# Kernel tuning notes

Measured on AMD Instinct MI355X. Metric: run time of the kernel, lower is better.

Reference implementation:

```python
import jax, jax.numpy as jnp
import numpy as np


def setup_inputs() -> dict:
    key = jax.random.key(0)
    k1, k2 = jax.random.split(key)
    N, I, J, K = 256, 32, 32, 256
    x = jax.random.normal(k1, (N, I, K), dtype=jnp.float32)
    z = jax.random.normal(k2, (N, J, K), dtype=jnp.float32)
    return {"x": x, "z": z}


def reference(x, z):
    # Original torch code loops over batch rolls; rolling only permutes the set
    # over which log_softmax (a permutation-invariant logsumexp) is taken, and
    # index 0 of the roll stack is always the diagonal pair (x[n], z[n]).
    # So it is exactly a symmetric InfoNCE over the full pairwise score matrix.
    J = z.shape[1]
    # Full pairwise token-level similarity: [N_x, N_z, I, J]
    sim = jnp.einsum('aik,bjk->abij', x, z)
    # score(x_a, z_b) = sum_{i,j} softmax_i(sim)*sim / J
    w = jax.nn.softmax(sim, axis=2) * sim
    S = w.sum(axis=(2, 3)) / J  # [N_x, N_z]
    diag = jnp.diagonal(S)
    # loss_x[n] = -log_softmax over x-candidates (axis 0) at the diagonal
    loss_x = jax.nn.logsumexp(S, axis=0) - diag
    # loss_z[n] = -log_softmax over z-candidates (axis 1) at the diagonal
    loss_z = jax.nn.logsumexp(S, axis=1) - diag
    loss = loss_x + loss_z
    return loss.mean()  # reduction='mean'
```

## Files before the change

kernel.cpp:

```cpp
#include <hip/hip_runtime.h>
#include <hip/hip_bf16.h>
#include <stdint.h>


typedef __attribute__((ext_vector_type(8))) short short8;
typedef __attribute__((ext_vector_type(16))) float float16;

#define NTOK 256
#define KDIM 256

__device__ __forceinline__ unsigned short f2bf(float f) {
    unsigned int u = __float_as_uint(f);
    unsigned int r = (u + 0x7fffu + ((u >> 16) & 1u)) >> 16;
    return (unsigned short)r;
}

__device__ __forceinline__ short8 cvt8(const float* p) {
    float4 f0 = ((const float4*)p)[0];
    float4 f1 = ((const float4*)p)[1];
    short8 v;
    v[0] = (short)f2bf(f0.x); v[1] = (short)f2bf(f0.y);
    v[2] = (short)f2bf(f0.z); v[3] = (short)f2bf(f0.w);
    v[4] = (short)f2bf(f1.x); v[5] = (short)f2bf(f1.y);
    v[6] = (short)f2bf(f1.z); v[7] = (short)f2bf(f1.w);
    return v;
}

__global__ void conv_kernel(const float* __restrict__ x,
                            const float* __restrict__ z,
                            short8* __restrict__ outbf,
                            float* __restrict__ out0) {
    const int uid = blockIdx.x * 256 + threadIdx.x;
    if (uid == 0) out0[0] = 0.0f;
    const int u = uid & 262143;
    const float* src = (uid < 262144) ? x : z;
    const int g  = u >> 10;
    const int r  = u & 1023;
    const int ks = r >> 6;
    const int h  = (r >> 5) & 1;
    const int l  = r & 31;
    outbf[uid] = cvt8(src + ((g * 32 + l) * KDIM + ks * 16 + h * 8));
}

template <bool F32SRC>
__global__ __launch_bounds__(256, 4)
void sim_kernel(const short8* __restrict__ xbf, const short8* __restrict__ zbf,
                const float* __restrict__ xf, const float* __restrict__ zf,
                float* __restrict__ S) {
    const int tid  = threadIdx.x;
    const int lane = tid & 63;
    const int wid  = tid >> 6;
    const int aw   = wid >> 1;
    const int bw   = wid & 1;
    const int l31  = lane & 31;
    const int half = lane >> 5;
    const int bid  = blockIdx.x;
    const int a0   = (bid >> 6) * 4;
    const int b0   = (bid & 63) * 4;

    const int ag = a0 + 2 * aw;
    const int bg = b0 + 2 * bw;

    const short8* pa = xbf + ag * 1024 + lane;
    const short8* pb = zbf + bg * 1024 + lane;

    const float* fa = xf + ((ag * 32 + l31) * KDIM + half * 8);
    const float* fb = zf + ((bg * 32 + l31) * KDIM + half * 8);

    float16 acc[2][2];
#pragma unroll
    for (int ai = 0; ai < 2; ai++)
#pragma unroll
        for (int bi = 0; bi < 2; bi++)
#pragma unroll
            for (int r = 0; r < 16; r++) acc[ai][bi][r] = 0.0f;

#pragma unroll 4
    for (int ks = 0; ks < 16; ks++) {
        short8 a0f, a1f, b0f, b1f;
        if (F32SRC) {
            a0f = cvt8(fa + ks * 16);
            a1f = cvt8(fa + 32 * KDIM + ks * 16);
            b0f = cvt8(fb + ks * 16);
            b1f = cvt8(fb + 32 * KDIM + ks * 16);
        } else {
            const int off = ks * 64;
            a0f = pa[off];
            a1f = pa[off + 1024];
            b0f = pb[off];
            b1f = pb[off + 1024];
        }
        acc[0][0] = __builtin_amdgcn_mfma_f32_32x32x16_bf16(a0f, b0f, acc[0][0], 0, 0, 0);
        acc[0][1] = __builtin_amdgcn_mfma_f32_32x32x16_bf16(a0f, b1f, acc[0][1], 0, 0, 0);
        acc[1][0] = __builtin_amdgcn_mfma_f32_32x32x16_bf16(a1f, b0f, acc[1][0], 0, 0, 0);
        acc[1][1] = __builtin_amdgcn_mfma_f32_32x32x16_bf16(a1f, b1f, acc[1][1], 0, 0, 0);
    }

#pragma unroll
    for (int ai = 0; ai < 2; ai++) {
#pragma unroll
        for (int bi = 0; bi < 2; bi++) {
            float16 c = acc[ai][bi];
            float m = c[0];
#pragma unroll
            for (int r = 1; r < 16; r++) m = fmaxf(m, c[r]);
            m = fmaxf(m, __shfl_xor(m, 32, 64));
            float se = 0.0f, swe = 0.0f;
#pragma unroll
            for (int r = 0; r < 16; r++) {
                float e = __expf(c[r] - m);
                se += e;
                swe = fmaf(e, c[r], swe);
            }
            se  += __shfl_xor(se, 32, 64);
            swe += __shfl_xor(swe, 32, 64);
            float cv = swe / se;
#pragma unroll
            for (int off = 1; off < 32; off <<= 1) cv += __shfl_xor(cv, off, 64);
            if (lane == 0)
                S[(ag + ai) * NTOK + (bg + bi)] = cv * (1.0f / 32.0f);
        }
    }
}

__global__ void loss_part(const float* __restrict__ S, float* __restrict__ out) {
    const int lane = threadIdx.x & 63;
    const int wid  = threadIdx.x >> 6;
    const int n    = blockIdx.x * 4 + wid;

    float cv[4], rv[4];
#pragma unroll
    for (int k = 0; k < 4; k++) {
        const int t = lane + 64 * k;
        cv[k] = S[t * NTOK + n];
        rv[k] = S[n * NTOK + t];
    }
    float m = fmaxf(fmaxf(cv[0], cv[1]), fmaxf(cv[2], cv[3]));
#pragma unroll
    for (int off = 1; off < 64; off <<= 1) m = fmaxf(m, __shfl_xor(m, off, 64));
    float s = 0.0f;
#pragma unroll
    for (int k = 0; k < 4; k++) s += __expf(cv[k] - m);
#pragma unroll
    for (int off = 1; off < 64; off <<= 1) s += __shfl_xor(s, off, 64);
    float lse_col = m + __logf(s);

    float m2 = fmaxf(fmaxf(rv[0], rv[1]), fmaxf(rv[2], rv[3]));
#pragma unroll
    for (int off = 1; off < 64; off <<= 1) m2 = fmaxf(m2, __shfl_xor(m2, off, 64));
    float s2 = 0.0f;
#pragma unroll
    for (int k = 0; k < 4; k++) s2 += __expf(rv[k] - m2);
#pragma unroll
    for (int off = 1; off < 64; off <<= 1) s2 += __shfl_xor(s2, off, 64);
    float lse_row = m2 + __logf(s2);

    __shared__ float red[4];
    if (lane == 0) {
        float diag = S[n * NTOK + n];
        red[wid] = (lse_col - diag) + (lse_row - diag);
    }
    __syncthreads();
    if (threadIdx.x == 0)
        atomicAdd(out, (red[0] + red[1] + red[2] + red[3]) * (1.0f / 256.0f));
}

__global__ void zero_kernel(float* __restrict__ out) {
    out[0] = 0.0f;
}

extern "C" void kernel_launch(void* const* d_in, const int* in_sizes, int n_in,
                              void* d_out, int out_size, void* d_ws, size_t ws_size,
                              hipStream_t stream) {
    const float* x = (const float*)d_in[0];
    const float* z = (const float*)d_in[1];
    float* out = (float*)d_out;

    const size_t bf_bytes = 524288ull * 16ull;
    const size_t s_bytes  = 256ull * 256ull * 4ull;

    if (ws_size >= bf_bytes + s_bytes) {
        short8* xbf = (short8*)d_ws;
        short8* zbf = xbf + 262144;
        float*  S   = (float*)((char*)d_ws + bf_bytes);
        conv_kernel<<<2048, 256, 0, stream>>>(x, z, (short8*)d_ws, out);
        sim_kernel<false><<<4096, 256, 0, stream>>>(xbf, zbf, nullptr, nullptr, S);
        loss_part<<<64, 256, 0, stream>>>(S, out);
    } else {
        float* S = (float*)d_ws;
        zero_kernel<<<1, 1, 0, stream>>>(out);
        sim_kernel<true><<<4096, 256, 0, stream>>>(nullptr, nullptr, x, z, S);
        loss_part<<<64, 256, 0, stream>>>(S, out);
    }
}
```

Before: 117.9 us.

## Defer cross-lane score reduction to a separate fp16 partial-sum kernel

Result: no change. 120.0 us (+1.8%).

```diff
diff --git a/kernel.cpp b/kernel.cpp
--- a/kernel.cpp
+++ b/kernel.cpp
@@ -1,5 +1,6 @@
 #include <hip/hip_runtime.h>
 #include <hip/hip_bf16.h>
+#include <hip/hip_fp16.h>
 #include <stdint.h>
 
 
@@ -42,11 +43,77 @@
     outbf[uid] = cvt8(src + ((g * 32 + l) * KDIM + ks * 16 + h * 8));
 }
 
-template <bool F32SRC>
+__device__ __forceinline__ void tile_epilogue_sp(const float16& c, __half* __restrict__ Sp,
+                                                 int a, int b, int lane) {
+    float m8[8], m4[4];
+#pragma unroll
+    for (int r = 0; r < 8; r++) m8[r] = fmaxf(c[2 * r], c[2 * r + 1]);
+#pragma unroll
+    for (int r = 0; r < 4; r++) m4[r] = fmaxf(m8[2 * r], m8[2 * r + 1]);
+    float m = fmaxf(fmaxf(m4[0], m4[1]), fmaxf(m4[2], m4[3]));
+    m = fmaxf(m, __shfl_xor(m, 32, 64));
+
+    float s0 = 0.f, s1 = 0.f, s2 = 0.f, s3 = 0.f;
+    float w0 = 0.f, w1 = 0.f, w2 = 0.f, w3 = 0.f;
+#pragma unroll
+    for (int r = 0; r < 16; r += 4) {
+        float e0 = __expf(c[r + 0] - m);
+        float e1 = __expf(c[r + 1] - m);
+        float e2 = __expf(c[r + 2] - m);
+        float e3 = __expf(c[r + 3] - m);
+        s0 += e0; s1 += e1; s2 += e2; s3 += e3;
+        w0 = fmaf(e0, c[r + 0], w0);
+        w1 = fmaf(e1, c[r + 1], w1);
+        w2 = fmaf(e2, c[r + 2], w2);
+        w3 = fmaf(e3, c[r + 3], w3);
+    }
+    float se  = (s0 + s1) + (s2 + s3);
+    float swe = (w0 + w1) + (w2 + w3);
+    se  += __shfl_xor(se, 32, 64);
+    swe += __shfl_xor(swe, 32, 64);
+    float cv = swe * __builtin_amdgcn_rcpf(se);
+    Sp[(((a << 8) + b) << 6) + lane] = __float2half_rn(cv);
+}
+
+__device__ __forceinline__ void tile_epilogue_bf(const float16& c, float* __restrict__ S,
+                                                 int a, int b, int lane) {
+    float m8[8], m4[4];
+#pragma unroll
+    for (int r = 0; r < 8; r++) m8[r] = fmaxf(c[2 * r], c[2 * r + 1]);
+#pragma unroll
+    for (int r = 0; r < 4; r++) m4[r] = fmaxf(m8[2 * r], m8[2 * r + 1]);
+    float m = fmaxf(fmaxf(m4[0], m4[1]), fmaxf(m4[2], m4[3]));
+    m = fmaxf(m, __shfl_xor(m, 32, 64));
+
+    float s0 = 0.f, s1 = 0.f, s2 = 0.f, s3 = 0.f;
+    float w0 = 0.f, w1 = 0.f, w2 = 0.f, w3 = 0.f;
+#pragma unroll
+    for (int r = 0; r < 16; r += 4) {
+        float e0 = __expf(c[r + 0] - m);
+        float e1 = __expf(c[r + 1] - m);
+        float e2 = __expf(c[r + 2] - m);
+        float e3 = __expf(c[r + 3] - m);
+        s0 += e0; s1 += e1; s2 += e2; s3 += e3;
+        w0 = fmaf(e0, c[r + 0], w0);
+        w1 = fmaf(e1, c[r + 1], w1);
+        w2 = fmaf(e2, c[r + 2], w2);
+        w3 = fmaf(e3, c[r + 3], w3);
+    }
+    float se  = (s0 + s1) + (s2 + s3);
+    float swe = (w0 + w1) + (w2 + w3);
+    se  += __shfl_xor(se, 32, 64);
+    swe += __shfl_xor(swe, 32, 64);
+    float cv = swe * __builtin_amdgcn_rcpf(se);
+#pragma unroll
+    for (int off = 1; off < 32; off <<= 1) cv += __shfl_xor(cv, off, 64);
+    if (lane == 0) S[a * NTOK + b] = cv * (1.0f / 32.0f);
+}
+
+template <bool F32SRC, bool SPSTORE>
 __global__ __launch_bounds__(256, 4)
 void sim_kernel(const short8* __restrict__ xbf, const short8* __restrict__ zbf,
                 const float* __restrict__ xf, const float* __restrict__ zf,
-                float* __restrict__ S) {
+                __half* __restrict__ Sp, float* __restrict__ S) {
     const int tid  = threadIdx.x;
     const int lane = tid & 63;
     const int wid  = tid >> 6;
@@ -97,30 +164,24 @@
     }
 
 #pragma unroll
-    for (int ai = 0; ai < 2; ai++) {
+    for (int ai = 0; ai < 2; ai++)
 #pragma unroll
         for (int bi = 0; bi < 2; bi++) {
-            float16 c = acc[ai][bi];
-            float m = c[0];
-#pragma unroll
-            for (int r = 1; r < 16; r++) m = fmaxf(m, c[r]);
-            m = fmaxf(m, __shfl_xor(m, 32, 64));
-            float se = 0.0f, swe = 0.0f;
-#pragma unroll
-            for (int r = 0; r < 16; r++) {
-                float e = __expf(c[r] - m);
-                se += e;
-                swe = fmaf(e, c[r], swe);
-            }
-            se  += __shfl_xor(se, 32, 64);
-            swe += __shfl_xor(swe, 32, 64);
-            float cv = swe / se;
-#pragma unroll
-            for (int off = 1; off < 32; off <<= 1) cv += __shfl_xor(cv, off, 64);
-            if (lane == 0)
-                S[(ag + ai) * NTOK + (bg + bi)] = cv * (1.0f / 32.0f);
+            if (SPSTORE) tile_epilogue_sp(acc[ai][bi], Sp, ag + ai, bg + bi, lane);
+            else         tile_epilogue_bf(acc[ai][bi], S,  ag + ai, bg + bi, lane);
         }
-    }
+}
+
+__global__ void red_kernel(const __half* __restrict__ Sp, float* __restrict__ S) {
+    const int t = blockIdx.x * 256 + threadIdx.x;
+    const __half2* h2 = (const __half2*)(Sp + (size_t)t * 64);
+    float s = 0.0f;
+#pragma unroll
+    for (int i = 0; i < 32; i++) {
+        float2 f = __half22float2(h2[i]);
+        s += f.x + f.y;
+    }
+    S[t] = s * (1.0f / 64.0f);
 }
 
 __global__ void loss_part(const float* __restrict__ S, float* __restrict__ out) {
@@ -177,19 +238,29 @@
     float* out = (float*)d_out;
 
     const size_t bf_bytes = 524288ull * 16ull;
+    const size_t sp_bytes = 65536ull * 64ull * 2ull;
     const size_t s_bytes  = 256ull * 256ull * 4ull;
 
-    if (ws_size >= bf_bytes + s_bytes) {
+    if (ws_size >= bf_bytes + sp_bytes + s_bytes) {
+        short8* xbf = (short8*)d_ws;
+        short8* zbf = xbf + 262144;
+        __half* Sp  = (__half*)((char*)d_ws + bf_bytes);
+        float*  S   = (float*)((char*)d_ws + bf_bytes + sp_bytes);
+        conv_kernel<<<2048, 256, 0, stream>>>(x, z, (short8*)d_ws, out);
+        sim_kernel<false, true><<<4096, 256, 0, stream>>>(xbf, zbf, nullptr, nullptr, Sp, S);
+        red_kernel<<<256, 256, 0, stream>>>(Sp, S);
+        loss_part<<<64, 256, 0, stream>>>(S, out);
+    } else if (ws_size >= bf_bytes + s_bytes) {
         short8* xbf = (short8*)d_ws;
         short8* zbf = xbf + 262144;
         float*  S   = (float*)((char*)d_ws + bf_bytes);
         conv_kernel<<<2048, 256, 0, stream>>>(x, z, (short8*)d_ws, out);
-        sim_kernel<false><<<4096, 256, 0, stream>>>(xbf, zbf, nullptr, nullptr, S);
+        sim_kernel<false, false><<<4096, 256, 0, stream>>>(xbf, zbf, nullptr, nullptr, nullptr, S);
         loss_part<<<64, 256, 0, stream>>>(S, out);
     } else {
         float* S = (float*)d_ws;
         zero_kernel<<<1, 1, 0, stream>>>(out);
-        sim_kernel<true><<<4096, 256, 0, stream>>>(nullptr, nullptr, x, z, S);
+        sim_kernel<true, false><<<4096, 256, 0, stream>>>(nullptr, nullptr, x, z, nullptr, S);
         loss_part<<<64, 256, 0, stream>>>(S, out);
     }
 }
```
